# Kernel tuning notes

Hardware: AMD Instinct MI355X
Metric: run time of the kernel (lower is better)

The kernel has to match this reference:

```python
import jax, jax.numpy as jnp
import numpy as np

SEQ = 256  # position axis length fixed by the graph's iota(256)


def _mod(freq, phase):
    # sin(2*pi*t*freq + phase)^2 * 0.1 + 1 - 0.05, shape [SEQ]
    t = jnp.arange(SEQ, dtype=jnp.float32)
    return jnp.sin(t * (2.0 * jnp.pi) * freq + phase) ** 2 * 0.1 + 0.95


def setup_inputs() -> dict:
    key = jax.random.key(0)
    ks = jax.random.split(key, 16)
    K = 2048  # number of scattered index triples
    return {
        "primals_1": jax.random.normal(ks[0], (6, 256, 256), jnp.float32),
        "primals_2": jax.random.normal(ks[1], (12, 6, 256), jnp.float32),
        "primals_3": jax.random.normal(ks[2], (6, 256, 256), jnp.float32),
        "primals_4": jax.random.normal(ks[3], (6, 256), jnp.float32),
        "primals_5": jax.random.randint(ks[4], (K,), 0, 6),
        "primals_6": jax.random.randint(ks[5], (K,), 0, 256),
        "primals_7": jax.random.randint(ks[6], (K,), 0, 256),
        "primals_8": jax.random.randint(ks[7], (K,), 0, 256),
        "primals_9": jax.random.uniform(ks[8], (1,), jnp.float32),
        "primals_10": jax.random.uniform(ks[9], (1,), jnp.float32),
        "primals_11": jax.random.normal(ks[10], (6, 256), jnp.float32),
        "primals_12": jax.random.uniform(ks[11], (1,), jnp.float32),
        "primals_13": jax.random.uniform(ks[12], (1,), jnp.float32),
        "primals_14": jax.random.normal(ks[13], (6, 256), jnp.float32),
        "primals_15": jax.random.uniform(ks[14], (1,), jnp.float32),
        "primals_16": jax.random.uniform(ks[15], (1,), jnp.float32),
    }


def reference(primals_1, primals_2, primals_3, primals_4, primals_5, primals_6,
              primals_7, primals_8, primals_9, primals_10, primals_11, primals_12,
              primals_13, primals_14, primals_15, primals_16):
    decay = primals_3 * 0.975  # reused in all three stages

    def stage(q, table, freq, phase):
        # gather from table [6,256] at (p5,p6) -> [K]
        vals = table[primals_5, primals_6]
        # scatter into a fresh copy of the persistent buffer, then decay-accumulate
        mem = primals_1.at[primals_5, primals_7, primals_8].set(vals) + decay  # [6,256,256]
        # bmm 'attention': q [12,6,256] x mem [6,256,256] -> [12,6,256]
        att = jnp.einsum('hbd,bde->hbe', q, mem)
        return att, _mod(freq, phase)

    a1, m1 = stage(primals_2, primals_4, primals_9, primals_10)
    x1 = a1 / m1
    a2, m2 = stage(x1, primals_11, primals_12, primals_13)
    x2 = a2 * m2
    a3, m3 = stage(x2, primals_14, primals_15, primals_16)
    return a3 / m3
```

## Files before the change

kernel.cpp:

```cpp
#include <hip/hip_runtime.h>

#define TWO_PI 6.2831853071795864769f


__global__ __launch_bounds__(1024) void prep_kernel(
    const float* __restrict__ P1, const float* __restrict__ P3,
    const int* __restrict__ p5, const int* __restrict__ p6,
    const int* __restrict__ p7, const int* __restrict__ p8,
    const float* __restrict__ T4, const float* __restrict__ T11,
    const float* __restrict__ T14,
    float* __restrict__ C, int* __restrict__ cnt,
    int* __restrict__ wde_g, float* __restrict__ wv_g, int K)
{
    const int tid = (int)threadIdx.x;
    const int blk = (int)blockIdx.x;
    if (blk < 96) {
        int i = blk * 1024 + tid;
        float4 a = ((const float4*)P1)[i];
        float4 c = ((const float4*)P3)[i];
        float4 r;
        r.x = fmaf(c.x, 0.975f, a.x);
        r.y = fmaf(c.y, 0.975f, a.y);
        r.z = fmaf(c.z, 0.975f, a.z);
        r.w = fmaf(c.w, 0.975f, a.w);
        ((float4*)C)[i] = r;
        return;
    }

    __shared__ unsigned pk[2048];
    __shared__ unsigned hmap[4096];
    __shared__ int scnt[8];
    for (int k = tid; k < K; k += 1024)
        pk[k] = ((unsigned)p5[k] << 24) | ((unsigned)p6[k] << 16) |
                ((unsigned)p7[k] << 8) | (unsigned)p8[k];
    for (int i = tid; i < 4096; i += 1024) hmap[i] = 0xFFFFFFFFu;
    if (tid < 8) scnt[tid] = 0;
    __syncthreads();

    for (int k = tid; k < K; k += 1024) {
        unsigned v = pk[k];
        unsigned key  = v & 0xFFFFu;
        unsigned full = (key << 3) | (v >> 24);
        unsigned mine = (full << 12) | (unsigned)k;
        unsigned hh = (full * 2654435761u) >> 20;
        for (;;) {
            unsigned prev = atomicCAS(&hmap[hh], 0xFFFFFFFFu, mine);
            if (prev == 0xFFFFFFFFu) break;
            if ((prev >> 12) == full) { atomicMax(&hmap[hh], mine); break; }
            hh = (hh + 1) & 4095u;
        }
    }
    __syncthreads();

    for (int k = tid; k < K; k += 1024) {
        unsigned v = pk[k];
        unsigned key  = v & 0xFFFFu;
        unsigned full = (key << 3) | (v >> 24);
        unsigned hh = (full * 2654435761u) >> 20;
        unsigned cur;
        for (;;) {
            cur = hmap[hh];
            if ((cur >> 12) == full) break;
            hh = (hh + 1) & 4095u;
        }
        if ((cur & 0xFFFu) == (unsigned)k) {
            int b = (int)(v >> 24), c = (int)((v >> 16) & 0xFFu);
            float p1v = P1[(b << 16) | key];
            int w = atomicAdd(&scnt[b], 1);
            wde_g[b * 2048 + w] = (int)key;
            wv_g[(0 * 6 + b) * 2048 + w] = T4 [b * 256 + c] - p1v;
            wv_g[(1 * 6 + b) * 2048 + w] = T11[b * 256 + c] - p1v;
            wv_g[(2 * 6 + b) * 2048 + w] = T14[b * 256 + c] - p1v;
        }
    }
    __syncthreads();
    if (tid < 8) cnt[tid] = scnt[tid];
}

__global__ __launch_bounds__(1024, 4) void chain_kernel(
    const float* __restrict__ C, const float* __restrict__ P2,
    const int* __restrict__ cnt, const int* __restrict__ wde_g,
    const float* __restrict__ wv_g,
    const float* __restrict__ f1, const float* __restrict__ ph1,
    const float* __restrict__ f2, const float* __restrict__ ph2,
    const float* __restrict__ f3, const float* __restrict__ ph3,
    float* __restrict__ out)
{
    __shared__ float vbuf[2][256];
    __shared__ float pv[16][256];
    __shared__ float modl[3][256];
    __shared__ int   wde[2048];
    __shared__ float wvs[3][2048];

    const int blk = (int)blockIdx.x;
    const int h = blk / 6, b = blk - h * 6;
    const int tid = (int)threadIdx.x;
    const int dg = tid >> 6, eg = tid & 63;

    const float4* Cv = (const float4*)C + (((b << 8) + (dg << 4)) << 6) + eg;
    float4 m4[16];
    #pragma unroll
    for (int i = 0; i < 16; ++i) m4[i] = Cv[i << 6];

    if (tid < 256) vbuf[0][tid] = P2[(h * 6 + b) * 256 + tid];
    if (tid < 768) {
        int s = tid >> 8, ee = tid & 255;
        float fr = (s == 0) ? f1[0]  : (s == 1) ? f2[0]  : f3[0];
        float ph = (s == 0) ? ph1[0] : (s == 1) ? ph2[0] : ph3[0];
        float sn = sinf((float)ee * TWO_PI * fr + ph);
        float mm = sn * sn * 0.1f + 0.95f;
        modl[s][ee] = (s == 1) ? mm : 1.0f / mm;
    }
    const int nwl = cnt[b];
    for (int i = tid; i < nwl; i += 1024) {
        wde[i]    = wde_g[b * 2048 + i];
        wvs[0][i] = wv_g[(0 * 6 + b) * 2048 + i];
        wvs[1][i] = wv_g[(1 * 6 + b) * 2048 + i];
        wvs[2][i] = wv_g[(2 * 6 + b) * 2048 + i];
    }
    __syncthreads();

    int cur = 0;
    for (int s = 0; s < 3; ++s) {
        const float* vin = vbuf[cur];
        float* vout = vbuf[cur ^ 1];
        float4 acc = make_float4(0.f, 0.f, 0.f, 0.f);
        #pragma unroll
        for (int j = 0; j < 4; ++j) {
            float4 vv = *(const float4*)&vin[(dg << 4) + (j << 2)];
            float4 m0 = m4[(j << 2) + 0];
            float4 m1 = m4[(j << 2) + 1];
            float4 m2 = m4[(j << 2) + 2];
            float4 m3 = m4[(j << 2) + 3];
            acc.x = fmaf(vv.x, m0.x, acc.x); acc.y = fmaf(vv.x, m0.y, acc.y);
            acc.z = fmaf(vv.x, m0.z, acc.z); acc.w = fmaf(vv.x, m0.w, acc.w);
            acc.x = fmaf(vv.y, m1.x, acc.x); acc.y = fmaf(vv.y, m1.y, acc.y);
            acc.z = fmaf(vv.y, m1.z, acc.z); acc.w = fmaf(vv.y, m1.w, acc.w);
            acc.x = fmaf(vv.z, m2.x, acc.x); acc.y = fmaf(vv.z, m2.y, acc.y);
            acc.z = fmaf(vv.z, m2.z, acc.z); acc.w = fmaf(vv.z, m2.w, acc.w);
            acc.x = fmaf(vv.w, m3.x, acc.x); acc.y = fmaf(vv.w, m3.y, acc.y);
            acc.z = fmaf(vv.w, m3.z, acc.z); acc.w = fmaf(vv.w, m3.w, acc.w);
        }
        *(float4*)&pv[dg][eg << 2] = acc;
        __syncthreads();
        if (tid < 256) {
            float x = 0.f;
            #pragma unroll
            for (int r = 0; r < 16; ++r) x += pv[r][tid];
            vout[tid] = x * modl[s][tid];
        }
        __syncthreads();
        for (int i = tid; i < nwl; i += 1024) {
            int de = wde[i];
            atomicAdd(&vout[de & 255],
                      vin[de >> 8] * wvs[s][i] * modl[s][de & 255]);
        }
        __syncthreads();
        cur ^= 1;
    }
    if (tid < 256) out[(h * 6 + b) * 256 + tid] = vbuf[cur][tid];
}

extern "C" void kernel_launch(void* const* d_in, const int* in_sizes, int n_in,
                              void* d_out, int out_size, void* d_ws, size_t ws_size,
                              hipStream_t stream)
{
    (void)n_in; (void)out_size; (void)ws_size;
    const float* P1  = (const float*)d_in[0];
    const float* P2  = (const float*)d_in[1];
    const float* P3  = (const float*)d_in[2];
    const float* T4  = (const float*)d_in[3];
    const int*   p5  = (const int*)d_in[4];
    const int*   p6  = (const int*)d_in[5];
    const int*   p7  = (const int*)d_in[6];
    const int*   p8  = (const int*)d_in[7];
    const float* f1  = (const float*)d_in[8];
    const float* ph1 = (const float*)d_in[9];
    const float* T11 = (const float*)d_in[10];
    const float* f2  = (const float*)d_in[11];
    const float* ph2 = (const float*)d_in[12];
    const float* T14 = (const float*)d_in[13];
    const float* f3  = (const float*)d_in[14];
    const float* ph3 = (const float*)d_in[15];
    float* out = (float*)d_out;
    int K = in_sizes[4];

    char* ws = (char*)d_ws;
    float* C     = (float*)(ws);
    int*   cnt   = (int*)  (ws + 1572864);
    int*   wde_g = (int*)  (ws + 1572928);
    float* wv_g  = (float*)(ws + 1622080);

    hipLaunchKernelGGL(prep_kernel, dim3(97), dim3(1024), 0, stream,
                       P1, P3, p5, p6, p7, p8, T4, T11, T14,
                       C, cnt, wde_g, wv_g, K);
    hipLaunchKernelGGL(chain_kernel, dim3(72), dim3(1024), 0, stream,
                       C, P2, cnt, wde_g, wv_g,
                       f1, ph1, f2, ph2, f3, ph3, out);
}
```

Baseline: 23.61 us.

## Reload C tile from global each stage instead of holding it in registers

Drops the 16 float4 register cache of the C tile and instead streams the tile from global memory (mostly L2-resident) inside each of the three stages. Two split accumulators are used, and the sin computation switches to the fast __sinf intrinsic. The launch-bounds occupancy hint is removed and the setup loads are reordered. This lowers register pressure and shortens the prologue before the first sync, but it triples global traffic for C and puts load latency on each stage's critical path. __sinf is also less accurate.

```diff
diff --git a/kernel.cpp b/kernel.cpp
--- a/kernel.cpp
+++ b/kernel.cpp
@@ -77,7 +77,7 @@
     if (tid < 8) cnt[tid] = scnt[tid];
 }
 
-__global__ __launch_bounds__(1024, 4) void chain_kernel(
+__global__ __launch_bounds__(1024) void chain_kernel(
     const float* __restrict__ C, const float* __restrict__ P2,
     const int* __restrict__ cnt, const int* __restrict__ wde_g,
     const float* __restrict__ wv_g,
@@ -97,20 +97,6 @@
     const int tid = (int)threadIdx.x;
     const int dg = tid >> 6, eg = tid & 63;
 
-    const float4* Cv = (const float4*)C + (((b << 8) + (dg << 4)) << 6) + eg;
-    float4 m4[16];
-    #pragma unroll
-    for (int i = 0; i < 16; ++i) m4[i] = Cv[i << 6];
-
-    if (tid < 256) vbuf[0][tid] = P2[(h * 6 + b) * 256 + tid];
-    if (tid < 768) {
-        int s = tid >> 8, ee = tid & 255;
-        float fr = (s == 0) ? f1[0]  : (s == 1) ? f2[0]  : f3[0];
-        float ph = (s == 0) ? ph1[0] : (s == 1) ? ph2[0] : ph3[0];
-        float sn = sinf((float)ee * TWO_PI * fr + ph);
-        float mm = sn * sn * 0.1f + 0.95f;
-        modl[s][ee] = (s == 1) ? mm : 1.0f / mm;
-    }
     const int nwl = cnt[b];
     for (int i = tid; i < nwl; i += 1024) {
         wde[i]    = wde_g[b * 2048 + i];
@@ -118,30 +104,37 @@
         wvs[1][i] = wv_g[(1 * 6 + b) * 2048 + i];
         wvs[2][i] = wv_g[(2 * 6 + b) * 2048 + i];
     }
+    if (tid < 256) vbuf[0][tid] = P2[(h * 6 + b) * 256 + tid];
+    if (tid < 768) {
+        int s = tid >> 8, ee = tid & 255;
+        float fr = (s == 0) ? f1[0]  : (s == 1) ? f2[0]  : f3[0];
+        float ph = (s == 0) ? ph1[0] : (s == 1) ? ph2[0] : ph3[0];
+        float sn = __sinf((float)ee * TWO_PI * fr + ph);
+        float mm = sn * sn * 0.1f + 0.95f;
+        modl[s][ee] = (s == 1) ? mm : 1.0f / mm;
+    }
     __syncthreads();
 
+    const float4* Cv = (const float4*)C + (((b << 8) + (dg << 4)) << 6) + eg;
     int cur = 0;
     for (int s = 0; s < 3; ++s) {
         const float* vin = vbuf[cur];
         float* vout = vbuf[cur ^ 1];
-        float4 acc = make_float4(0.f, 0.f, 0.f, 0.f);
+        float4 a0 = make_float4(0.f, 0.f, 0.f, 0.f);
+        float4 a1 = make_float4(0.f, 0.f, 0.f, 0.f);
         #pragma unroll
-        for (int j = 0; j < 4; ++j) {
-            float4 vv = *(const float4*)&vin[(dg << 4) + (j << 2)];
-            float4 m0 = m4[(j << 2) + 0];
-            float4 m1 = m4[(j << 2) + 1];
-            float4 m2 = m4[(j << 2) + 2];
-            float4 m3 = m4[(j << 2) + 3];
-            acc.x = fmaf(vv.x, m0.x, acc.x); acc.y = fmaf(vv.x, m0.y, acc.y);
-            acc.z = fmaf(vv.x, m0.z, acc.z); acc.w = fmaf(vv.x, m0.w, acc.w);
-            acc.x = fmaf(vv.y, m1.x, acc.x); acc.y = fmaf(vv.y, m1.y, acc.y);
-            acc.z = fmaf(vv.y, m1.z, acc.z); acc.w = fmaf(vv.y, m1.w, acc.w);
-            acc.x = fmaf(vv.z, m2.x, acc.x); acc.y = fmaf(vv.z, m2.y, acc.y);
-            acc.z = fmaf(vv.z, m2.z, acc.z); acc.w = fmaf(vv.z, m2.w, acc.w);
-            acc.x = fmaf(vv.w, m3.x, acc.x); acc.y = fmaf(vv.w, m3.y, acc.y);
-            acc.z = fmaf(vv.w, m3.z, acc.z); acc.w = fmaf(vv.w, m3.w, acc.w);
+        for (int i = 0; i < 16; i += 2) {
+            float4 c0 = Cv[i << 6];
+            float4 c1 = Cv[(i + 1) << 6];
+            float v0 = vin[(dg << 4) + i];
+            float v1 = vin[(dg << 4) + i + 1];
+            a0.x = fmaf(v0, c0.x, a0.x); a0.y = fmaf(v0, c0.y, a0.y);
+            a0.z = fmaf(v0, c0.z, a0.z); a0.w = fmaf(v0, c0.w, a0.w);
+            a1.x = fmaf(v1, c1.x, a1.x); a1.y = fmaf(v1, c1.y, a1.y);
+            a1.z = fmaf(v1, c1.z, a1.z); a1.w = fmaf(v1, c1.w, a1.w);
         }
-        *(float4*)&pv[dg][eg << 2] = acc;
+        a0.x += a1.x; a0.y += a1.y; a0.z += a1.z; a0.w += a1.w;
+        *(float4*)&pv[dg][eg << 2] = a0;
         __syncthreads();
         if (tid < 256) {
             float x = 0.f;
```

New measurement: 25.93 us. +9.8%, slower.
